# Kernel optimization log

Hardware: AMD Instinct MI355X
Metric: run time of the kernel (lower is better)

Reference implementation:

```python
import jax, jax.numpy as jnp
import numpy as np

SEQ, BATCH, H = 512, 1024, 64  # hidden == input == 64 (8x8 grid)


def setup_inputs() -> dict:
    key = jax.random.key(0)
    k_x, k_wih, k_whh, k_bih, k_bhh = jax.random.split(key, 5)
    s = 1.0 / np.sqrt(H)  # PyTorch LSTM init scale U(-1/sqrt(H), 1/sqrt(H))
    x = jax.random.normal(k_x, (SEQ, BATCH, 8, 8), dtype=jnp.float32)
    W_ih = jax.random.uniform(k_wih, (4 * H, H), jnp.float32, -s, s)
    W_hh = jax.random.uniform(k_whh, (4 * H, H), jnp.float32, -s, s)
    b_ih = jax.random.uniform(k_bih, (4 * H,), jnp.float32, -s, s)
    b_hh = jax.random.uniform(k_bhh, (4 * H,), jnp.float32, -s, s)
    return {"x": x, "W_ih": W_ih, "W_hh": W_hh, "b_ih": b_ih, "b_hh": b_hh}


def _lstm(x_flat, W_ih, W_hh, b_ih, b_hh):
    # x_flat: (seq, batch, H). PyTorch gate order: i, f, g, o.
    seq, batch, _ = x_flat.shape
    # Precompute input projections for all timesteps in one big GEMM.
    xg = jnp.einsum('sbh,gh->sbg', x_flat, W_ih) + (b_ih + b_hh)  # (seq, batch, 4H)

    def step(carry, xg_t):
        h, c = carry
        gates = xg_t + h @ W_hh.T  # (batch, 4H)
        i, f, g, o = jnp.split(gates, 4, axis=-1)
        i = jax.nn.sigmoid(i)
        f = jax.nn.sigmoid(f)
        g = jnp.tanh(g)
        o = jax.nn.sigmoid(o)
        c = f * c + i * g
        h = o * jnp.tanh(c)
        return (h, c), h

    h0 = jnp.zeros((batch, W_hh.shape[1]), x_flat.dtype)
    c0 = jnp.zeros_like(h0)
    _, hs = jax.lax.scan(step, (h0, c0), xg)
    return hs  # (seq, batch, H)


def reference(x, W_ih, W_hh, b_ih, b_hh):
    seq, batch = x.shape[0], x.shape[1]
    x_flat = x.reshape(seq, batch, 64)  # Flatten(start_dim=2)
    hs = _lstm(x_flat, W_ih, W_hh, b_ih, b_hh)
    return hs.reshape(-1, 1024, 8, 8)
```

## Files before the change

### kernel.cpp

```cpp
#include <hip/hip_runtime.h>
#include <hip/hip_bf16.h>

#define SEQ   512
#define BATCH 1024
#define HD    64
#define NS    4
#define TCH   64
#define XPAD  80

typedef __attribute__((ext_vector_type(8))) short bf16x8;
typedef __attribute__((ext_vector_type(4))) float f32x4;

__device__ __forceinline__ unsigned short f2bf(float f) {
    unsigned u = __float_as_uint(f);
    return (unsigned short)((u + 0x7FFFu + ((u >> 16) & 1u)) >> 16);
}
__device__ __forceinline__ float frcp(float x) { return __builtin_amdgcn_rcpf(x); }
__device__ __forceinline__ float fsig(float x) { return frcp(1.f + __expf(-x)); }
__device__ __forceinline__ float ftanh(float x) { return 1.f - 2.f * frcp(__expf(2.f * x) + 1.f); }

__global__ __launch_bounds__(256, 1)
void lstm_v6(const float* __restrict__ x,
             const float* __restrict__ W_ih,
             const float* __restrict__ W_hh,
             const float* __restrict__ b_ih,
             const float* __restrict__ b_hh,
             float* __restrict__ out)
{
    __shared__ __align__(16) unsigned short xch[TCH][NS][XPAD];
    __shared__ __align__(16) unsigned short hb[2][NS][XPAD];

    const int tid  = threadIdx.x;
    const int w    = tid >> 6;
    const int ln   = tid & 63;
    const int col  = ln & 15;
    const int kg   = ln >> 4;
    const int slot = (ln >> 2) & 3;
    const int q    = ln >> 4;
    const int unit = w * 16 + col;
    const int sBase = blockIdx.x * NS;

    bf16x8 bfr[4][4];
    #pragma unroll
    for (int g4 = 0; g4 < 4; ++g4) {
        #pragma unroll
        for (int kt = 0; kt < 4; ++kt) {
            const int n = (g4 * 4 + w) * 16 + col;
            const int k = kt * 32 + kg * 8;
            const float* src = (k < 64) ? (W_ih + n * 64 + k)
                                        : (W_hh + n * 64 + (k - 64));
            const float4 lo = *(const float4*)src;
            const float4 hi = *(const float4*)(src + 4);
            bf16x8 v;
            v[0] = (short)f2bf(lo.x); v[1] = (short)f2bf(lo.y);
            v[2] = (short)f2bf(lo.z); v[3] = (short)f2bf(lo.w);
            v[4] = (short)f2bf(hi.x); v[5] = (short)f2bf(hi.y);
            v[6] = (short)f2bf(hi.z); v[7] = (short)f2bf(hi.w);
            bfr[g4][kt] = v;
        }
    }
    float bs[4];
    #pragma unroll
    for (int g4 = 0; g4 < 4; ++g4)
        bs[g4] = b_ih[g4 * 64 + unit] + b_hh[g4 * 64 + unit];

    for (int i = tid; i < (2 * NS * XPAD) / 2; i += 256) ((unsigned*)hb)[i] = 0;

    float c_st = 0.f;
    int p = 0;
    float* outp = out + (size_t)(sBase + q) * HD + unit;
    const f32x4 z4 = {0.f, 0.f, 0.f, 0.f};

    for (int t0 = 0; t0 < SEQ; t0 += TCH) {
        #pragma unroll
        for (int j = 0; j < (TCH * NS * 16) / 256; ++j) {
            const int idx = tid + j * 256;
            const int k4 = idx & 15, sl = (idx >> 4) & 3, tt = idx >> 6;
            const float4 v = *(const float4*)&x[(((size_t)(t0 + tt) * BATCH) + sBase + sl) * HD + k4 * 4];
            uint2 pk;
            pk.x = (unsigned)f2bf(v.x) | ((unsigned)f2bf(v.y) << 16);
            pk.y = (unsigned)f2bf(v.z) | ((unsigned)f2bf(v.w) << 16);
            *(uint2*)&xch[tt][sl][k4 * 4] = pk;
        }
        __syncthreads();

        bf16x8 ax0 = *(const bf16x8*)&xch[0][slot][kg * 8];
        bf16x8 ax1 = *(const bf16x8*)&xch[0][slot][32 + kg * 8];

        for (int tc = 0; tc < TCH; ++tc) {
            const int t = t0 + tc;
            const bf16x8 ah0 = *(const bf16x8*)&hb[p][slot][kg * 8];
            const bf16x8 ah1 = *(const bf16x8*)&hb[p][slot][32 + kg * 8];

            f32x4 xa0 = __builtin_amdgcn_mfma_f32_16x16x32_bf16(ax0, bfr[0][0], z4, 0, 0, 0);
            f32x4 xa1 = __builtin_amdgcn_mfma_f32_16x16x32_bf16(ax0, bfr[1][0], z4, 0, 0, 0);
            f32x4 xa2 = __builtin_amdgcn_mfma_f32_16x16x32_bf16(ax0, bfr[2][0], z4, 0, 0, 0);
            f32x4 xa3 = __builtin_amdgcn_mfma_f32_16x16x32_bf16(ax0, bfr[3][0], z4, 0, 0, 0);
            xa0 = __builtin_amdgcn_mfma_f32_16x16x32_bf16(ax1, bfr[0][1], xa0, 0, 0, 0);
            xa1 = __builtin_amdgcn_mfma_f32_16x16x32_bf16(ax1, bfr[1][1], xa1, 0, 0, 0);
            xa2 = __builtin_amdgcn_mfma_f32_16x16x32_bf16(ax1, bfr[2][1], xa2, 0, 0, 0);
            xa3 = __builtin_amdgcn_mfma_f32_16x16x32_bf16(ax1, bfr[3][1], xa3, 0, 0, 0);
            f32x4 ha0 = __builtin_amdgcn_mfma_f32_16x16x32_bf16(ah0, bfr[0][2], z4, 0, 0, 0);
            f32x4 ha1 = __builtin_amdgcn_mfma_f32_16x16x32_bf16(ah0, bfr[1][2], z4, 0, 0, 0);
            f32x4 ha2 = __builtin_amdgcn_mfma_f32_16x16x32_bf16(ah0, bfr[2][2], z4, 0, 0, 0);
            f32x4 ha3 = __builtin_amdgcn_mfma_f32_16x16x32_bf16(ah0, bfr[3][2], z4, 0, 0, 0);
            ha0 = __builtin_amdgcn_mfma_f32_16x16x32_bf16(ah1, bfr[0][3], ha0, 0, 0, 0);
            ha1 = __builtin_amdgcn_mfma_f32_16x16x32_bf16(ah1, bfr[1][3], ha1, 0, 0, 0);
            ha2 = __builtin_amdgcn_mfma_f32_16x16x32_bf16(ah1, bfr[2][3], ha2, 0, 0, 0);
            ha3 = __builtin_amdgcn_mfma_f32_16x16x32_bf16(ah1, bfr[3][3], ha3, 0, 0, 0);

            bf16x8 nx0 = ax0, nx1 = ax1;
            if (tc + 1 < TCH) {
                nx0 = *(const bf16x8*)&xch[tc + 1][slot][kg * 8];
                nx1 = *(const bf16x8*)&xch[tc + 1][slot][32 + kg * 8];
            }

            const float gi = xa0[0] + ha0[0] + bs[0];
            const float gf = xa1[0] + ha1[0] + bs[1];
            const float gg = xa2[0] + ha2[0] + bs[2];
            const float go = xa3[0] + ha3[0] + bs[3];
            const float iv = fsig(gi);
            const float fv = fsig(gf);
            const float gv = ftanh(gg);
            const float ov = fsig(go);
            c_st = fv * c_st + iv * gv;
            const float h  = ov * ftanh(c_st);
            outp[(size_t)t * (BATCH * HD)] = h;
            hb[p ^ 1][q][unit] = f2bf(h);

            ax0 = nx0; ax1 = nx1;
            p ^= 1;
            __syncthreads();
        }
    }
}

extern "C" void kernel_launch(void* const* d_in, const int* in_sizes, int n_in,
                              void* d_out, int out_size, void* d_ws, size_t ws_size,
                              hipStream_t stream) {
    const float* x    = (const float*)d_in[0];
    const float* W_ih = (const float*)d_in[1];
    const float* W_hh = (const float*)d_in[2];
    const float* b_ih = (const float*)d_in[3];
    const float* b_hh = (const float*)d_in[4];
    float* out = (float*)d_out;

    lstm_v6<<<BATCH / NS, 256, 0, stream>>>(x, W_ih, W_hh, b_ih, b_hh, out);
}
```

Before: 181.2 us.

## Split LSTM block into recurrent and producer wavefronts with double-buffered input chunks

Doubles the block to 512 threads. Four wavefronts run only the recurrent h·W_hh MFMAs and the gate math, while four producer wavefronts precompute the next step's x·W_ih plus bias into shared memory, double-buffer the input chunk loads, and write the previous step's h to global memory. This takes the input projection, the global loads and the output stores off the serial critical path. The recurrent waves also raise their scheduling priority around the MFMAs. In exchange it adds shared-memory traffic and keeps a block-wide barrier every step across twice as many waves.

```diff
diff --git a/kernel.cpp b/kernel.cpp
--- a/kernel.cpp
+++ b/kernel.cpp
@@ -19,16 +19,18 @@
 __device__ __forceinline__ float fsig(float x) { return frcp(1.f + __expf(-x)); }
 __device__ __forceinline__ float ftanh(float x) { return 1.f - 2.f * frcp(__expf(2.f * x) + 1.f); }
 
-__global__ __launch_bounds__(256, 1)
-void lstm_v6(const float* __restrict__ x,
+__global__ __launch_bounds__(512, 1)
+void lstm_v8(const float* __restrict__ x,
              const float* __restrict__ W_ih,
              const float* __restrict__ W_hh,
              const float* __restrict__ b_ih,
              const float* __restrict__ b_hh,
              float* __restrict__ out)
 {
-    __shared__ __align__(16) unsigned short xch[TCH][NS][XPAD];
+    __shared__ __align__(16) unsigned short xch[2][TCH][NS][XPAD];
+    __shared__ __align__(16) float          xg[2][NS][HD][4];
     __shared__ __align__(16) unsigned short hb[2][NS][XPAD];
+    __shared__ __align__(16) float          hf[2][NS][HD + 4];
 
     const int tid  = threadIdx.x;
     const int w    = tid >> 6;
@@ -37,20 +39,21 @@
     const int kg   = ln >> 4;
     const int slot = (ln >> 2) & 3;
     const int q    = ln >> 4;
-    const int unit = w * 16 + col;
     const int sBase = blockIdx.x * NS;
+    const bool isH = (w < 4);
+    const int u    = isH ? w : (w - 4);
+    const int unit = u * 16 + col;
 
-    bf16x8 bfr[4][4];
+    const float* Wsrc = isH ? W_hh : W_ih;
+    bf16x8 bfr[4][2];
     #pragma unroll
     for (int g4 = 0; g4 < 4; ++g4) {
         #pragma unroll
-        for (int kt = 0; kt < 4; ++kt) {
-            const int n = (g4 * 4 + w) * 16 + col;
+        for (int kt = 0; kt < 2; ++kt) {
+            const int n = (g4 * 4 + u) * 16 + col;
             const int k = kt * 32 + kg * 8;
-            const float* src = (k < 64) ? (W_ih + n * 64 + k)
-                                        : (W_hh + n * 64 + (k - 64));
-            const float4 lo = *(const float4*)src;
-            const float4 hi = *(const float4*)(src + 4);
+            const float4 lo = *(const float4*)(Wsrc + n * 64 + k);
+            const float4 hi = *(const float4*)(Wsrc + n * 64 + k + 4);
             bf16x8 v;
             v[0] = (short)f2bf(lo.x); v[1] = (short)f2bf(lo.y);
             v[2] = (short)f2bf(lo.z); v[3] = (short)f2bf(lo.w);
@@ -59,80 +62,90 @@
             bfr[g4][kt] = v;
         }
     }
-    float bs[4];
+    f32x4 bias4[4];
     #pragma unroll
-    for (int g4 = 0; g4 < 4; ++g4)
-        bs[g4] = b_ih[g4 * 64 + unit] + b_hh[g4 * 64 + unit];
+    for (int g4 = 0; g4 < 4; ++g4) {
+        const float b = isH ? 0.f : (b_ih[g4 * 64 + unit] + b_hh[g4 * 64 + unit]);
+        bias4[g4][0] = b; bias4[g4][1] = b; bias4[g4][2] = b; bias4[g4][3] = b;
+    }
 
-    for (int i = tid; i < (2 * NS * XPAD) / 2; i += 256) ((unsigned*)hb)[i] = 0;
+    for (int i = tid; i < (2 * NS * XPAD) / 2; i += 512) ((unsigned*)hb)[i] = 0;
+
+    const int L = (w - 4) * 64 + ln;
+    const int qq = (L >> 6) & 3, uu = L & 63;
+
+    auto refill = [&](int C, int b) {
+        #pragma unroll
+        for (int j = 0; j < 16; ++j) {
+            const int idx = L + j * 256;
+            const int k4 = idx & 15, sl = (idx >> 4) & 3, tt = idx >> 6;
+            const float4 v = *(const float4*)&x[(((size_t)(C * TCH + tt) * BATCH) + sBase + sl) * HD + k4 * 4];
+            uint2 pk;
+            pk.x = (unsigned)f2bf(v.x) | ((unsigned)f2bf(v.y) << 16);
+            pk.y = (unsigned)f2bf(v.z) | ((unsigned)f2bf(v.w) << 16);
+            *(uint2*)&xch[b][tt][sl][k4 * 4] = pk;
+        }
+    };
+    auto produce = [&](int tn) {
+        const int cb = (tn >> 6) & 1, tc = tn & 63;
+        const bf16x8 ax0 = *(const bf16x8*)&xch[cb][tc][slot][kg * 8];
+        const bf16x8 ax1 = *(const bf16x8*)&xch[cb][tc][slot][32 + kg * 8];
+        f32x4 a0 = __builtin_amdgcn_mfma_f32_16x16x32_bf16(ax0, bfr[0][0], bias4[0], 0, 0, 0);
+        f32x4 a1 = __builtin_amdgcn_mfma_f32_16x16x32_bf16(ax0, bfr[1][0], bias4[1], 0, 0, 0);
+        f32x4 a2 = __builtin_amdgcn_mfma_f32_16x16x32_bf16(ax0, bfr[2][0], bias4[2], 0, 0, 0);
+        f32x4 a3 = __builtin_amdgcn_mfma_f32_16x16x32_bf16(ax0, bfr[3][0], bias4[3], 0, 0, 0);
+        a0 = __builtin_amdgcn_mfma_f32_16x16x32_bf16(ax1, bfr[0][1], a0, 0, 0, 0);
+        a1 = __builtin_amdgcn_mfma_f32_16x16x32_bf16(ax1, bfr[1][1], a1, 0, 0, 0);
+        a2 = __builtin_amdgcn_mfma_f32_16x16x32_bf16(ax1, bfr[2][1], a2, 0, 0, 0);
+        a3 = __builtin_amdgcn_mfma_f32_16x16x32_bf16(ax1, bfr[3][1], a3, 0, 0, 0);
+        f32x4 v; v[0] = a0[0]; v[1] = a1[0]; v[2] = a2[0]; v[3] = a3[0];
+        *(f32x4*)&xg[tn & 1][q][unit][0] = v;
+    };
+
+    if (!isH) refill(0, 0);
+    __syncthreads();
+    if (!isH) produce(0);
+    __syncthreads();
 
     float c_st = 0.f;
     int p = 0;
-    float* outp = out + (size_t)(sBase + q) * HD + unit;
     const f32x4 z4 = {0.f, 0.f, 0.f, 0.f};
 
-    for (int t0 = 0; t0 < SEQ; t0 += TCH) {
-        #pragma unroll
-        for (int j = 0; j < (TCH * NS * 16) / 256; ++j) {
-            const int idx = tid + j * 256;
-            const int k4 = idx & 15, sl = (idx >> 4) & 3, tt = idx >> 6;
-            const float4 v = *(const float4*)&x[(((size_t)(t0 + tt) * BATCH) + sBase + sl) * HD + k4 * 4];
-            uint2 pk;
-            pk.x = (unsigned)f2bf(v.x) | ((unsigned)f2bf(v.y) << 16);
-            pk.y = (unsigned)f2bf(v.z) | ((unsigned)f2bf(v.w) << 16);
-            *(uint2*)&xch[tt][sl][k4 * 4] = pk;
-        }
-        __syncthreads();
-
-        bf16x8 ax0 = *(const bf16x8*)&xch[0][slot][kg * 8];
-        bf16x8 ax1 = *(const bf16x8*)&xch[0][slot][32 + kg * 8];
-
-        for (int tc = 0; tc < TCH; ++tc) {
-            const int t = t0 + tc;
+    for (int t = 0; t < SEQ; ++t) {
+        if (isH) {
             const bf16x8 ah0 = *(const bf16x8*)&hb[p][slot][kg * 8];
             const bf16x8 ah1 = *(const bf16x8*)&hb[p][slot][32 + kg * 8];
-
-            f32x4 xa0 = __builtin_amdgcn_mfma_f32_16x16x32_bf16(ax0, bfr[0][0], z4, 0, 0, 0);
-            f32x4 xa1 = __builtin_amdgcn_mfma_f32_16x16x32_bf16(ax0, bfr[1][0], z4, 0, 0, 0);
-            f32x4 xa2 = __builtin_amdgcn_mfma_f32_16x16x32_bf16(ax0, bfr[2][0], z4, 0, 0, 0);
-            f32x4 xa3 = __builtin_amdgcn_mfma_f32_16x16x32_bf16(ax0, bfr[3][0], z4, 0, 0, 0);
-            xa0 = __builtin_amdgcn_mfma_f32_16x16x32_bf16(ax1, bfr[0][1], xa0, 0, 0, 0);
-            xa1 = __builtin_amdgcn_mfma_f32_16x16x32_bf16(ax1, bfr[1][1], xa1, 0, 0, 0);
-            xa2 = __builtin_amdgcn_mfma_f32_16x16x32_bf16(ax1, bfr[2][1], xa2, 0, 0, 0);
-            xa3 = __builtin_amdgcn_mfma_f32_16x16x32_bf16(ax1, bfr[3][1], xa3, 0, 0, 0);
-            f32x4 ha0 = __builtin_amdgcn_mfma_f32_16x16x32_bf16(ah0, bfr[0][2], z4, 0, 0, 0);
-            f32x4 ha1 = __builtin_amdgcn_mfma_f32_16x16x32_bf16(ah0, bfr[1][2], z4, 0, 0, 0);
-            f32x4 ha2 = __builtin_amdgcn_mfma_f32_16x16x32_bf16(ah0, bfr[2][2], z4, 0, 0, 0);
-            f32x4 ha3 = __builtin_amdgcn_mfma_f32_16x16x32_bf16(ah0, bfr[3][2], z4, 0, 0, 0);
-            ha0 = __builtin_amdgcn_mfma_f32_16x16x32_bf16(ah1, bfr[0][3], ha0, 0, 0, 0);
-            ha1 = __builtin_amdgcn_mfma_f32_16x16x32_bf16(ah1, bfr[1][3], ha1, 0, 0, 0);
-            ha2 = __builtin_amdgcn_mfma_f32_16x16x32_bf16(ah1, bfr[2][3], ha2, 0, 0, 0);
-            ha3 = __builtin_amdgcn_mfma_f32_16x16x32_bf16(ah1, bfr[3][3], ha3, 0, 0, 0);
-
-            bf16x8 nx0 = ax0, nx1 = ax1;
-            if (tc + 1 < TCH) {
-                nx0 = *(const bf16x8*)&xch[tc + 1][slot][kg * 8];
-                nx1 = *(const bf16x8*)&xch[tc + 1][slot][32 + kg * 8];
-            }
-
-            const float gi = xa0[0] + ha0[0] + bs[0];
-            const float gf = xa1[0] + ha1[0] + bs[1];
-            const float gg = xa2[0] + ha2[0] + bs[2];
-            const float go = xa3[0] + ha3[0] + bs[3];
-            const float iv = fsig(gi);
-            const float fv = fsig(gf);
-            const float gv = ftanh(gg);
-            const float ov = fsig(go);
+            const f32x4  xgv = *(const f32x4*)&xg[t & 1][q][unit][0];
+            __builtin_amdgcn_s_setprio(1);
+            f32x4 a0 = __builtin_amdgcn_mfma_f32_16x16x32_bf16(ah0, bfr[0][0], z4, 0, 0, 0);
+            f32x4 a1 = __builtin_amdgcn_mfma_f32_16x16x32_bf16(ah0, bfr[1][0], z4, 0, 0, 0);
+            f32x4 a2 = __builtin_amdgcn_mfma_f32_16x16x32_bf16(ah0, bfr[2][0], z4, 0, 0, 0);
+            f32x4 a3 = __builtin_amdgcn_mfma_f32_16x16x32_bf16(ah0, bfr[3][0], z4, 0, 0, 0);
+            a0 = __builtin_amdgcn_mfma_f32_16x16x32_bf16(ah1, bfr[0][1], a0, 0, 0, 0);
+            a1 = __builtin_amdgcn_mfma_f32_16x16x32_bf16(ah1, bfr[1][1], a1, 0, 0, 0);
+            a2 = __builtin_amdgcn_mfma_f32_16x16x32_bf16(ah1, bfr[2][1], a2, 0, 0, 0);
+            a3 = __builtin_amdgcn_mfma_f32_16x16x32_bf16(ah1, bfr[3][1], a3, 0, 0, 0);
+            __builtin_amdgcn_s_setprio(0);
+            const float iv = fsig(xgv[0] + a0[0]);
+            const float fv = fsig(xgv[1] + a1[0]);
+            const float gv = ftanh(xgv[2] + a2[0]);
+            const float ov = fsig(xgv[3] + a3[0]);
             c_st = fv * c_st + iv * gv;
-            const float h  = ov * ftanh(c_st);
-            outp[(size_t)t * (BATCH * HD)] = h;
+            const float h = ov * ftanh(c_st);
             hb[p ^ 1][q][unit] = f2bf(h);
-
-            ax0 = nx0; ax1 = nx1;
-            p ^= 1;
-            __syncthreads();
+            hf[p ^ 1][q][unit] = h;
+        } else {
+            if ((t & 63) == 0 && t + TCH < SEQ)
+                refill((t >> 6) + 1, ((t >> 6) + 1) & 1);
+            if (t + 1 < SEQ) produce(t + 1);
+            if (t >= 1)
+                out[((size_t)(t - 1) * BATCH + sBase + qq) * HD + uu] = hf[p][qq][uu];
         }
+        p ^= 1;
+        __syncthreads();
     }
+    if (!isH)
+        out[((size_t)(SEQ - 1) * BATCH + sBase + qq) * HD + uu] = hf[p][qq][uu];
 }
 
 extern "C" void kernel_launch(void* const* d_in, const int* in_sizes, int n_in,
@@ -145,5 +158,5 @@
     const float* b_hh = (const float*)d_in[4];
     float* out = (float*)d_out;
 
-    lstm_v6<<<BATCH / NS, 256, 0, stream>>>(x, W_ih, W_hh, b_ih, b_hh, out);
+    lstm_v8<<<BATCH / NS, 512, 0, stream>>>(x, W_ih, W_hh, b_ih, b_hh, out);
 }
```

Result: slower. 186.2 us (+2.8%).

## Map one batch sample per single-wave block and batch input projection per 16 steps

Applied to the files above, without the earlier changes.

Replaces the 4-wave block handling 4 samples with a 1024-block grid of single 64-lane waves, each owning one batch sample. The input projection for 16 timesteps is now done in one batch of MFMAs and staged through LDS. Each step then runs only the recurrent MFMAs, holding all weights in registers. Because a block is a single wave, the per-step __syncthreads disappears. In exchange each wave issues 32 MFMAs per step, with most of the 16 rows unused, and register pressure rises sharply from keeping all Bx/Bh fragments resident.

```diff
diff --git a/kernel.cpp b/kernel.cpp
--- a/kernel.cpp
+++ b/kernel.cpp
@@ -4,9 +4,6 @@
 #define SEQ   512
 #define BATCH 1024
 #define HD    64
-#define NS    4
-#define TCH   64
-#define XPAD  80
 
 typedef __attribute__((ext_vector_type(8))) short bf16x8;
 typedef __attribute__((ext_vector_type(4))) float f32x4;
@@ -19,118 +16,109 @@
 __device__ __forceinline__ float fsig(float x) { return frcp(1.f + __expf(-x)); }
 __device__ __forceinline__ float ftanh(float x) { return 1.f - 2.f * frcp(__expf(2.f * x) + 1.f); }
 
-__global__ __launch_bounds__(256, 1)
-void lstm_v6(const float* __restrict__ x,
+__global__ __launch_bounds__(64, 1)
+void lstm_v9(const float* __restrict__ x,
              const float* __restrict__ W_ih,
              const float* __restrict__ W_hh,
              const float* __restrict__ b_ih,
              const float* __restrict__ b_hh,
              float* __restrict__ out)
 {
-    __shared__ __align__(16) unsigned short xch[TCH][NS][XPAD];
-    __shared__ __align__(16) unsigned short hb[2][NS][XPAD];
+    __shared__ __align__(16) unsigned short xch[16][72];
+    __shared__ __align__(16) float xg[16][16][17];
+    __shared__ __align__(16) unsigned short hbuf[64];
 
-    const int tid  = threadIdx.x;
-    const int w    = tid >> 6;
-    const int ln   = tid & 63;
-    const int col  = ln & 15;
-    const int kg   = ln >> 4;
-    const int slot = (ln >> 2) & 3;
-    const int q    = ln >> 4;
-    const int unit = w * 16 + col;
-    const int sBase = blockIdx.x * NS;
+    const int l  = threadIdx.x;
+    const int cl = l & 15;
+    const int kg = l >> 4;
+    const int s  = blockIdx.x;
 
-    bf16x8 bfr[4][4];
+    bf16x8 Bx[16][2], Bh[16][2];
     #pragma unroll
-    for (int g4 = 0; g4 < 4; ++g4) {
+    for (int j = 0; j < 16; ++j) {
         #pragma unroll
-        for (int kt = 0; kt < 4; ++kt) {
-            const int n = (g4 * 4 + w) * 16 + col;
+        for (int kt = 0; kt < 2; ++kt) {
+            const int n = j * 16 + cl;
             const int k = kt * 32 + kg * 8;
-            const float* src = (k < 64) ? (W_ih + n * 64 + k)
-                                        : (W_hh + n * 64 + (k - 64));
-            const float4 lo = *(const float4*)src;
-            const float4 hi = *(const float4*)(src + 4);
-            bf16x8 v;
-            v[0] = (short)f2bf(lo.x); v[1] = (short)f2bf(lo.y);
-            v[2] = (short)f2bf(lo.z); v[3] = (short)f2bf(lo.w);
-            v[4] = (short)f2bf(hi.x); v[5] = (short)f2bf(hi.y);
-            v[6] = (short)f2bf(hi.z); v[7] = (short)f2bf(hi.w);
-            bfr[g4][kt] = v;
+            const float4 a0 = *(const float4*)(W_ih + n * 64 + k);
+            const float4 a1 = *(const float4*)(W_ih + n * 64 + k + 4);
+            const float4 b0 = *(const float4*)(W_hh + n * 64 + k);
+            const float4 b1 = *(const float4*)(W_hh + n * 64 + k + 4);
+            bf16x8 vx, vh;
+            vx[0]=(short)f2bf(a0.x); vx[1]=(short)f2bf(a0.y); vx[2]=(short)f2bf(a0.z); vx[3]=(short)f2bf(a0.w);
+            vx[4]=(short)f2bf(a1.x); vx[5]=(short)f2bf(a1.y); vx[6]=(short)f2bf(a1.z); vx[7]=(short)f2bf(a1.w);
+            vh[0]=(short)f2bf(b0.x); vh[1]=(short)f2bf(b0.y); vh[2]=(short)f2bf(b0.z); vh[3]=(short)f2bf(b0.w);
+            vh[4]=(short)f2bf(b1.x); vh[5]=(short)f2bf(b1.y); vh[6]=(short)f2bf(b1.z); vh[7]=(short)f2bf(b1.w);
+            Bx[j][kt] = vx; Bh[j][kt] = vh;
         }
     }
     float bs[4];
     #pragma unroll
-    for (int g4 = 0; g4 < 4; ++g4)
-        bs[g4] = b_ih[g4 * 64 + unit] + b_hh[g4 * 64 + unit];
+    for (int g = 0; g < 4; ++g) bs[g] = b_ih[g * 64 + l] + b_hh[g * 64 + l];
 
-    for (int i = tid; i < (2 * NS * XPAD) / 2; i += 256) ((unsigned*)hb)[i] = 0;
+    if (l < 32) ((unsigned*)hbuf)[l] = 0;
 
     float c_st = 0.f;
-    int p = 0;
-    float* outp = out + (size_t)(sBase + q) * HD + unit;
+    float* outp = out + (size_t)s * HD + l;
     const f32x4 z4 = {0.f, 0.f, 0.f, 0.f};
 
-    for (int t0 = 0; t0 < SEQ; t0 += TCH) {
+    for (int T = 0; T < SEQ; T += 16) {
         #pragma unroll
-        for (int j = 0; j < (TCH * NS * 16) / 256; ++j) {
-            const int idx = tid + j * 256;
-            const int k4 = idx & 15, sl = (idx >> 4) & 3, tt = idx >> 6;
-            const float4 v = *(const float4*)&x[(((size_t)(t0 + tt) * BATCH) + sBase + sl) * HD + k4 * 4];
+        for (int j = 0; j < 4; ++j) {
+            const int idx = j * 64 + l;
+            const int tt = idx >> 4, k4 = idx & 15;
+            const float4 v = *(const float4*)&x[((size_t)(T + tt) * BATCH + s) * HD + k4 * 4];
             uint2 pk;
             pk.x = (unsigned)f2bf(v.x) | ((unsigned)f2bf(v.y) << 16);
             pk.y = (unsigned)f2bf(v.z) | ((unsigned)f2bf(v.w) << 16);
-            *(uint2*)&xch[tt][sl][k4 * 4] = pk;
+            *(uint2*)&xch[tt][k4 * 4] = pk;
         }
-        __syncthreads();
+        {
+            const bf16x8 axp0 = *(const bf16x8*)&xch[cl][kg * 8];
+            const bf16x8 axp1 = *(const bf16x8*)&xch[cl][32 + kg * 8];
+            #pragma unroll
+            for (int j = 0; j < 16; ++j) {
+                f32x4 a = __builtin_amdgcn_mfma_f32_16x16x32_bf16(axp0, Bx[j][0], z4, 0, 0, 0);
+                a = __builtin_amdgcn_mfma_f32_16x16x32_bf16(axp1, Bx[j][1], a, 0, 0, 0);
+                *(f32x4*)&xg[j][cl][kg * 4] = a;
+            }
+        }
+        for (int tc = 0; tc < 16; ++tc) {
+            const int t = T + tc;
+            const float xgi = xg[kg][cl][tc];
+            const float xgf = xg[4 + kg][cl][tc];
+            const float xgg = xg[8 + kg][cl][tc];
+            const float xgo = xg[12 + kg][cl][tc];
+            const bf16x8 ah0 = *(const bf16x8*)&hbuf[kg * 8];
+            const bf16x8 ah1 = *(const bf16x8*)&hbuf[32 + kg * 8];
 
-        bf16x8 ax0 = *(const bf16x8*)&xch[0][slot][kg * 8];
-        bf16x8 ax1 = *(const bf16x8*)&xch[0][slot][32 + kg * 8];
+            f32x4 acc[16];
+            #pragma unroll
+            for (int j = 0; j < 16; ++j)
+                acc[j] = __builtin_amdgcn_mfma_f32_16x16x32_bf16(ah0, Bh[j][0], z4, 0, 0, 0);
+            #pragma unroll
+            for (int j = 0; j < 16; ++j)
+                acc[j] = __builtin_amdgcn_mfma_f32_16x16x32_bf16(ah1, Bh[j][1], acc[j], 0, 0, 0);
 
-        for (int tc = 0; tc < TCH; ++tc) {
-            const int t = t0 + tc;
-            const bf16x8 ah0 = *(const bf16x8*)&hb[p][slot][kg * 8];
-            const bf16x8 ah1 = *(const bf16x8*)&hb[p][slot][32 + kg * 8];
+            const bool s1 = (kg & 1), s2 = (kg & 2);
+            const float i01 = s1 ? acc[1][0]  : acc[0][0],  i23 = s1 ? acc[3][0]  : acc[2][0];
+            const float f01 = s1 ? acc[5][0]  : acc[4][0],  f23 = s1 ? acc[7][0]  : acc[6][0];
+            const float g01 = s1 ? acc[9][0]  : acc[8][0],  g23 = s1 ? acc[11][0] : acc[10][0];
+            const float o01 = s1 ? acc[13][0] : acc[12][0], o23 = s1 ? acc[15][0] : acc[14][0];
+            const float gi = (s2 ? i23 : i01) + xgi + bs[0];
+            const float gf = (s2 ? f23 : f01) + xgf + bs[1];
+            const float gg = (s2 ? g23 : g01) + xgg + bs[2];
+            const float go = (s2 ? o23 : o01) + xgo + bs[3];
 
-            f32x4 xa0 = __builtin_amdgcn_mfma_f32_16x16x32_bf16(ax0, bfr[0][0], z4, 0, 0, 0);
-            f32x4 xa1 = __builtin_amdgcn_mfma_f32_16x16x32_bf16(ax0, bfr[1][0], z4, 0, 0, 0);
-            f32x4 xa2 = __builtin_amdgcn_mfma_f32_16x16x32_bf16(ax0, bfr[2][0], z4, 0, 0, 0);
-            f32x4 xa3 = __builtin_amdgcn_mfma_f32_16x16x32_bf16(ax0, bfr[3][0], z4, 0, 0, 0);
-            xa0 = __builtin_amdgcn_mfma_f32_16x16x32_bf16(ax1, bfr[0][1], xa0, 0, 0, 0);
-            xa1 = __builtin_amdgcn_mfma_f32_16x16x32_bf16(ax1, bfr[1][1], xa1, 0, 0, 0);
-            xa2 = __builtin_amdgcn_mfma_f32_16x16x32_bf16(ax1, bfr[2][1], xa2, 0, 0, 0);
-            xa3 = __builtin_amdgcn_mfma_f32_16x16x32_bf16(ax1, bfr[3][1], xa3, 0, 0, 0);
-            f32x4 ha0 = __builtin_amdgcn_mfma_f32_16x16x32_bf16(ah0, bfr[0][2], z4, 0, 0, 0);
-            f32x4 ha1 = __builtin_amdgcn_mfma_f32_16x16x32_bf16(ah0, bfr[1][2], z4, 0, 0, 0);
-            f32x4 ha2 = __builtin_amdgcn_mfma_f32_16x16x32_bf16(ah0, bfr[2][2], z4, 0, 0, 0);
-            f32x4 ha3 = __builtin_amdgcn_mfma_f32_16x16x32_bf16(ah0, bfr[3][2], z4, 0, 0, 0);
-            ha0 = __builtin_amdgcn_mfma_f32_16x16x32_bf16(ah1, bfr[0][3], ha0, 0, 0, 0);
-            ha1 = __builtin_amdgcn_mfma_f32_16x16x32_bf16(ah1, bfr[1][3], ha1, 0, 0, 0);
-            ha2 = __builtin_amdgcn_mfma_f32_16x16x32_bf16(ah1, bfr[2][3], ha2, 0, 0, 0);
-            ha3 = __builtin_amdgcn_mfma_f32_16x16x32_bf16(ah1, bfr[3][3], ha3, 0, 0, 0);
-
-            bf16x8 nx0 = ax0, nx1 = ax1;
-            if (tc + 1 < TCH) {
-                nx0 = *(const bf16x8*)&xch[tc + 1][slot][kg * 8];
-                nx1 = *(const bf16x8*)&xch[tc + 1][slot][32 + kg * 8];
-            }
-
-            const float gi = xa0[0] + ha0[0] + bs[0];
-            const float gf = xa1[0] + ha1[0] + bs[1];
-            const float gg = xa2[0] + ha2[0] + bs[2];
-            const float go = xa3[0] + ha3[0] + bs[3];
             const float iv = fsig(gi);
             const float fv = fsig(gf);
             const float gv = ftanh(gg);
             const float ov = fsig(go);
             c_st = fv * c_st + iv * gv;
             const float h  = ov * ftanh(c_st);
+
             outp[(size_t)t * (BATCH * HD)] = h;
-            hb[p ^ 1][q][unit] = f2bf(h);
-
-            ax0 = nx0; ax1 = nx1;
-            p ^= 1;
-            __syncthreads();
+            hbuf[l] = f2bf(h);
         }
     }
 }
@@ -145,5 +133,5 @@
     const float* b_hh = (const float*)d_in[4];
     float* out = (float*)d_out;
 
-    lstm_v6<<<BATCH / NS, 256, 0, stream>>>(x, W_ih, W_hh, b_ih, b_hh, out);
+    lstm_v9<<<BATCH, 64, 0, stream>>>(x, W_ih, W_hh, b_ih, b_hh, out);
 }
```

Measured after the change: 342.6 us. +89.1%, slower.

## Halve sequences per block and batch input projections per time tile

Applied to the files above, without the earlier changes.

Each block now handles two sequences instead of four, which doubles the grid, and launch bounds allow two blocks per CU. The input projection is taken off the recurrent critical path: for every 16-step tile it is computed with MFMA over all timesteps into an fp32 LDS buffer, so each recurrent step runs only the 8 hidden-state MFMAs at raised wave priority. This shortens the serial per-step dependency chain and adds parallelism, but leaves half of each wave idle in the gate math and adds an LDS round trip for the precomputed gates.

```diff
diff --git a/kernel.cpp b/kernel.cpp
--- a/kernel.cpp
+++ b/kernel.cpp
@@ -4,9 +4,8 @@
 #define SEQ   512
 #define BATCH 1024
 #define HD    64
-#define NS    4
-#define TCH   64
-#define XPAD  80
+#define NS    2
+#define TB    16
 
 typedef __attribute__((ext_vector_type(8))) short bf16x8;
 typedef __attribute__((ext_vector_type(4))) float f32x4;
@@ -19,64 +18,66 @@
 __device__ __forceinline__ float fsig(float x) { return frcp(1.f + __expf(-x)); }
 __device__ __forceinline__ float ftanh(float x) { return 1.f - 2.f * frcp(__expf(2.f * x) + 1.f); }
 
-__global__ __launch_bounds__(256, 1)
-void lstm_v6(const float* __restrict__ x,
-             const float* __restrict__ W_ih,
-             const float* __restrict__ W_hh,
-             const float* __restrict__ b_ih,
-             const float* __restrict__ b_hh,
-             float* __restrict__ out)
+__global__ __launch_bounds__(256, 2)
+void lstm_v10(const float* __restrict__ x,
+              const float* __restrict__ W_ih,
+              const float* __restrict__ W_hh,
+              const float* __restrict__ b_ih,
+              const float* __restrict__ b_hh,
+              float* __restrict__ out)
 {
-    __shared__ __align__(16) unsigned short xch[TCH][NS][XPAD];
-    __shared__ __align__(16) unsigned short hb[2][NS][XPAD];
+    __shared__ __align__(16) unsigned short xch[TB][NS][72];
+    __shared__ __align__(16) float xg[NS][16][16][18];
+    __shared__ __align__(16) unsigned short hb[2][NS][80];
 
     const int tid  = threadIdx.x;
     const int w    = tid >> 6;
     const int ln   = tid & 63;
     const int col  = ln & 15;
     const int kg   = ln >> 4;
-    const int slot = (ln >> 2) & 3;
+    const int slot = (ln >> 2) & 1;
     const int q    = ln >> 4;
+    const int qc   = q & 1;
     const int unit = w * 16 + col;
     const int sBase = blockIdx.x * NS;
 
-    bf16x8 bfr[4][4];
+    bf16x8 Bx[4][2], Bh[4][2];
     #pragma unroll
-    for (int g4 = 0; g4 < 4; ++g4) {
+    for (int g = 0; g < 4; ++g) {
         #pragma unroll
-        for (int kt = 0; kt < 4; ++kt) {
-            const int n = (g4 * 4 + w) * 16 + col;
+        for (int kt = 0; kt < 2; ++kt) {
+            const int n = (g * 4 + w) * 16 + col;
             const int k = kt * 32 + kg * 8;
-            const float* src = (k < 64) ? (W_ih + n * 64 + k)
-                                        : (W_hh + n * 64 + (k - 64));
-            const float4 lo = *(const float4*)src;
-            const float4 hi = *(const float4*)(src + 4);
-            bf16x8 v;
-            v[0] = (short)f2bf(lo.x); v[1] = (short)f2bf(lo.y);
-            v[2] = (short)f2bf(lo.z); v[3] = (short)f2bf(lo.w);
-            v[4] = (short)f2bf(hi.x); v[5] = (short)f2bf(hi.y);
-            v[6] = (short)f2bf(hi.z); v[7] = (short)f2bf(hi.w);
-            bfr[g4][kt] = v;
+            const float4 xa = *(const float4*)(W_ih + n * 64 + k);
+            const float4 xb = *(const float4*)(W_ih + n * 64 + k + 4);
+            const float4 ha = *(const float4*)(W_hh + n * 64 + k);
+            const float4 hbq = *(const float4*)(W_hh + n * 64 + k + 4);
+            bf16x8 vx, vh;
+            vx[0]=(short)f2bf(xa.x); vx[1]=(short)f2bf(xa.y); vx[2]=(short)f2bf(xa.z); vx[3]=(short)f2bf(xa.w);
+            vx[4]=(short)f2bf(xb.x); vx[5]=(short)f2bf(xb.y); vx[6]=(short)f2bf(xb.z); vx[7]=(short)f2bf(xb.w);
+            vh[0]=(short)f2bf(ha.x); vh[1]=(short)f2bf(ha.y); vh[2]=(short)f2bf(ha.z); vh[3]=(short)f2bf(ha.w);
+            vh[4]=(short)f2bf(hbq.x); vh[5]=(short)f2bf(hbq.y); vh[6]=(short)f2bf(hbq.z); vh[7]=(short)f2bf(hbq.w);
+            Bx[g][kt] = vx; Bh[g][kt] = vh;
         }
     }
     float bs[4];
     #pragma unroll
-    for (int g4 = 0; g4 < 4; ++g4)
-        bs[g4] = b_ih[g4 * 64 + unit] + b_hh[g4 * 64 + unit];
+    for (int g = 0; g < 4; ++g)
+        bs[g] = b_ih[g * 64 + unit] + b_hh[g * 64 + unit];
 
-    for (int i = tid; i < (2 * NS * XPAD) / 2; i += 256) ((unsigned*)hb)[i] = 0;
+    if (tid < 160) ((unsigned*)hb)[tid] = 0;
 
     float c_st = 0.f;
     int p = 0;
-    float* outp = out + (size_t)(sBase + q) * HD + unit;
     const f32x4 z4 = {0.f, 0.f, 0.f, 0.f};
+    float* outp = out + (size_t)(sBase + qc) * HD + unit;
 
-    for (int t0 = 0; t0 < SEQ; t0 += TCH) {
+    for (int T = 0; T < SEQ; T += TB) {
         #pragma unroll
-        for (int j = 0; j < (TCH * NS * 16) / 256; ++j) {
+        for (int j = 0; j < 2; ++j) {
             const int idx = tid + j * 256;
-            const int k4 = idx & 15, sl = (idx >> 4) & 3, tt = idx >> 6;
-            const float4 v = *(const float4*)&x[(((size_t)(t0 + tt) * BATCH) + sBase + sl) * HD + k4 * 4];
+            const int k4 = idx & 15, sl = (idx >> 4) & 1, tt = idx >> 5;
+            const float4 v = *(const float4*)&x[(((size_t)(T + tt) * BATCH) + sBase + sl) * HD + k4 * 4];
             uint2 pk;
             pk.x = (unsigned)f2bf(v.x) | ((unsigned)f2bf(v.y) << 16);
             pk.y = (unsigned)f2bf(v.z) | ((unsigned)f2bf(v.w) << 16);
@@ -84,51 +85,52 @@
         }
         __syncthreads();
 
-        bf16x8 ax0 = *(const bf16x8*)&xch[0][slot][kg * 8];
-        bf16x8 ax1 = *(const bf16x8*)&xch[0][slot][32 + kg * 8];
+        #pragma unroll
+        for (int m = 0; m < NS; ++m) {
+            const bf16x8 a0 = *(const bf16x8*)&xch[ln & 15][m][kg * 8];
+            const bf16x8 a1 = *(const bf16x8*)&xch[ln & 15][m][32 + kg * 8];
+            #pragma unroll
+            for (int g = 0; g < 4; ++g) {
+                f32x4 a = __builtin_amdgcn_mfma_f32_16x16x32_bf16(a0, Bx[g][0], z4, 0, 0, 0);
+                a = __builtin_amdgcn_mfma_f32_16x16x32_bf16(a1, Bx[g][1], a, 0, 0, 0);
+                *(f32x4*)&xg[m][g * 4 + w][col][4 * kg] = a;
+            }
+        }
 
-        for (int tc = 0; tc < TCH; ++tc) {
-            const int t = t0 + tc;
+        for (int tc = 0; tc < TB; ++tc) {
+            const int t = T + tc;
+            const float xgi = xg[qc][0 * 4 + w][col][tc];
+            const float xgf = xg[qc][1 * 4 + w][col][tc];
+            const float xgg = xg[qc][2 * 4 + w][col][tc];
+            const float xgo = xg[qc][3 * 4 + w][col][tc];
             const bf16x8 ah0 = *(const bf16x8*)&hb[p][slot][kg * 8];
             const bf16x8 ah1 = *(const bf16x8*)&hb[p][slot][32 + kg * 8];
 
-            f32x4 xa0 = __builtin_amdgcn_mfma_f32_16x16x32_bf16(ax0, bfr[0][0], z4, 0, 0, 0);
-            f32x4 xa1 = __builtin_amdgcn_mfma_f32_16x16x32_bf16(ax0, bfr[1][0], z4, 0, 0, 0);
-            f32x4 xa2 = __builtin_amdgcn_mfma_f32_16x16x32_bf16(ax0, bfr[2][0], z4, 0, 0, 0);
-            f32x4 xa3 = __builtin_amdgcn_mfma_f32_16x16x32_bf16(ax0, bfr[3][0], z4, 0, 0, 0);
-            xa0 = __builtin_amdgcn_mfma_f32_16x16x32_bf16(ax1, bfr[0][1], xa0, 0, 0, 0);
-            xa1 = __builtin_amdgcn_mfma_f32_16x16x32_bf16(ax1, bfr[1][1], xa1, 0, 0, 0);
-            xa2 = __builtin_amdgcn_mfma_f32_16x16x32_bf16(ax1, bfr[2][1], xa2, 0, 0, 0);
-            xa3 = __builtin_amdgcn_mfma_f32_16x16x32_bf16(ax1, bfr[3][1], xa3, 0, 0, 0);
-            f32x4 ha0 = __builtin_amdgcn_mfma_f32_16x16x32_bf16(ah0, bfr[0][2], z4, 0, 0, 0);
-            f32x4 ha1 = __builtin_amdgcn_mfma_f32_16x16x32_bf16(ah0, bfr[1][2], z4, 0, 0, 0);
-            f32x4 ha2 = __builtin_amdgcn_mfma_f32_16x16x32_bf16(ah0, bfr[2][2], z4, 0, 0, 0);
-            f32x4 ha3 = __builtin_amdgcn_mfma_f32_16x16x32_bf16(ah0, bfr[3][2], z4, 0, 0, 0);
-            ha0 = __builtin_amdgcn_mfma_f32_16x16x32_bf16(ah1, bfr[0][3], ha0, 0, 0, 0);
-            ha1 = __builtin_amdgcn_mfma_f32_16x16x32_bf16(ah1, bfr[1][3], ha1, 0, 0, 0);
-            ha2 = __builtin_amdgcn_mfma_f32_16x16x32_bf16(ah1, bfr[2][3], ha2, 0, 0, 0);
-            ha3 = __builtin_amdgcn_mfma_f32_16x16x32_bf16(ah1, bfr[3][3], ha3, 0, 0, 0);
+            __builtin_amdgcn_s_setprio(1);
+            f32x4 a0 = __builtin_amdgcn_mfma_f32_16x16x32_bf16(ah0, Bh[0][0], z4, 0, 0, 0);
+            f32x4 a1 = __builtin_amdgcn_mfma_f32_16x16x32_bf16(ah0, Bh[1][0], z4, 0, 0, 0);
+            f32x4 a2 = __builtin_amdgcn_mfma_f32_16x16x32_bf16(ah0, Bh[2][0], z4, 0, 0, 0);
+            f32x4 a3 = __builtin_amdgcn_mfma_f32_16x16x32_bf16(ah0, Bh[3][0], z4, 0, 0, 0);
+            a0 = __builtin_amdgcn_mfma_f32_16x16x32_bf16(ah1, Bh[0][1], a0, 0, 0, 0);
+            a1 = __builtin_amdgcn_mfma_f32_16x16x32_bf16(ah1, Bh[1][1], a1, 0, 0, 0);
+            a2 = __builtin_amdgcn_mfma_f32_16x16x32_bf16(ah1, Bh[2][1], a2, 0, 0, 0);
+            a3 = __builtin_amdgcn_mfma_f32_16x16x32_bf16(ah1, Bh[3][1], a3, 0, 0, 0);
+            __builtin_amdgcn_s_setprio(0);
 
-            bf16x8 nx0 = ax0, nx1 = ax1;
-            if (tc + 1 < TCH) {
-                nx0 = *(const bf16x8*)&xch[tc + 1][slot][kg * 8];
-                nx1 = *(const bf16x8*)&xch[tc + 1][slot][32 + kg * 8];
+            if (ln < 32) {
+                const float gi = xgi + a0[0] + bs[0];
+                const float gf = xgf + a1[0] + bs[1];
+                const float gg = xgg + a2[0] + bs[2];
+                const float go = xgo + a3[0] + bs[3];
+                const float iv = fsig(gi);
+                const float fv = fsig(gf);
+                const float gv = ftanh(gg);
+                const float ov = fsig(go);
+                c_st = fv * c_st + iv * gv;
+                const float h  = ov * ftanh(c_st);
+                outp[(size_t)t * (BATCH * HD)] = h;
+                hb[p ^ 1][q][unit] = f2bf(h);
             }
-
-            const float gi = xa0[0] + ha0[0] + bs[0];
-            const float gf = xa1[0] + ha1[0] + bs[1];
-            const float gg = xa2[0] + ha2[0] + bs[2];
-            const float go = xa3[0] + ha3[0] + bs[3];
-            const float iv = fsig(gi);
-            const float fv = fsig(gf);
-            const float gv = ftanh(gg);
-            const float ov = fsig(go);
-            c_st = fv * c_st + iv * gv;
-            const float h  = ov * ftanh(c_st);
-            outp[(size_t)t * (BATCH * HD)] = h;
-            hb[p ^ 1][q][unit] = f2bf(h);
-
-            ax0 = nx0; ax1 = nx1;
             p ^= 1;
             __syncthreads();
         }
@@ -145,5 +147,5 @@
     const float* b_hh = (const float*)d_in[4];
     float* out = (float*)d_out;
 
-    lstm_v6<<<BATCH / NS, 256, 0, stream>>>(x, W_ih, W_hh, b_ih, b_hh, out);
+    lstm_v10<<<BATCH / NS, 256, 0, stream>>>(x, W_ih, W_hh, b_ih, b_hh, out);
 }
```

Measured after the change: 191.1 us. 1.05x slower.
